# Kernel tuning notes

Hardware: AMD Instinct MI355X
Metric: run time of the kernel (lower is better)

## Reference

```python
import jax, jax.numpy as jnp
import numpy as np

Z_DIM = 128
OUT_DIM = 64
CHANNELS = 3
N_LINEARS = 16
BATCH = 1024
OUT_FEATS = CHANNELS * OUT_DIM * OUT_DIM * N_LINEARS  # 196608


def setup_inputs() -> dict:
    key = jax.random.key(0)
    k_z, k_c, k_w, k_b = jax.random.split(key, 4)
    z = jax.random.normal(k_z, (BATCH, Z_DIM), dtype=jnp.float32)
    # torch.randint(0, n_linears - 1, ...) -> values in [0, 14]
    c = jax.random.randint(k_c, (BATCH,), 0, N_LINEARS - 1, dtype=jnp.int64)
    W = jax.random.normal(k_w, (OUT_FEATS, Z_DIM), dtype=jnp.float32) * 0.02
    b = jax.random.normal(k_b, (OUT_FEATS,), dtype=jnp.float32) * 0.02
    return {"z": z, "c": c, "W": W, "b": b}


def reference(z, c, W, b):
    # Dense linear producing n_linears 'expert' outputs per sample
    out = jnp.einsum('bz,oz->bo', z, W) + b               # [B, O*N]
    out = out.reshape(-1, N_LINEARS, CHANNELS, OUT_DIM, OUT_DIM)
    # Per-sample gather of the selected expert slice
    return out[jnp.arange(out.shape[0]), c]               # [B, C, H, W]
```

## Files before the change

### kernel.cpp

```cpp
#include <hip/hip_runtime.h>


#define Z_DIM  128
#define OPE    12288
#define NEXP   16
#define NT     256
#define NCOLS  128
#define MCHUNK 64
#define WPAD   136

typedef __attribute__((ext_vector_type(8))) short short8;
typedef __attribute__((ext_vector_type(4))) float f32x4;
typedef unsigned short u16;
typedef unsigned int   u32;

__device__ __forceinline__ u16 f2bf(float f) {
    union { float f; u32 u; } a; a.f = f;
    const u32 r = a.u + 0x7FFFu + ((a.u >> 16) & 1u);
    return (u16)(r >> 16);
}

__global__ __launch_bounds__(NT, 6)
void expert_mfma(const float* __restrict__ z,
                 const int* __restrict__ c,
                 const float* __restrict__ W,
                 const float* __restrict__ bias,
                 float* __restrict__ out,
                 int B) {
    __shared__ u16 lst[1024];
    __shared__ int cnt_sh;
    __shared__ __align__(16) u16 Zhi[MCHUNK][WPAD];

    const int tid = threadIdx.x;
    const int e   = blockIdx.y;
    const int n0  = blockIdx.x * NCOLS;

    if (tid == 0) cnt_sh = 0;
    __syncthreads();
    {
        const int4 cv = ((const int4*)c)[tid];
        if (cv.x == e) lst[atomicAdd(&cnt_sh, 1)] = (u16)(tid * 4 + 0);
        if (cv.y == e) lst[atomicAdd(&cnt_sh, 1)] = (u16)(tid * 4 + 1);
        if (cv.z == e) lst[atomicAdd(&cnt_sh, 1)] = (u16)(tid * 4 + 2);
        if (cv.w == e) lst[atomicAdd(&cnt_sh, 1)] = (u16)(tid * 4 + 3);
    }
    __syncthreads();
    const int cnt = cnt_sh;
    if (cnt == 0) return;

    const int lane = tid & 63;
    const int wv   = tid >> 6;
    const int fr   = lane & 15;
    const int kg   = lane >> 4;

    const int col0 = n0 + wv * 16 + fr;
    const int col1 = col0 + 64;
    const float bv0 = bias[(size_t)e * OPE + col0];
    const float bv1 = bias[(size_t)e * OPE + col1];

    short8 bh0[4], bh1[4];
    #pragma unroll
    for (int cg = 0; cg < 2; ++cg) {
        const float* wrow = W + ((size_t)e * OPE + (cg ? col1 : col0)) * Z_DIM;
        #pragma unroll
        for (int kk = 0; kk < 4; ++kk) {
            const float* p = wrow + kk * 32 + kg * 8;
            const float4 v0 = *(const float4*)p;
            const float4 v1 = *(const float4*)(p + 4);
            short8 hh;
            hh[0]=(short)f2bf(v0.x); hh[1]=(short)f2bf(v0.y);
            hh[2]=(short)f2bf(v0.z); hh[3]=(short)f2bf(v0.w);
            hh[4]=(short)f2bf(v1.x); hh[5]=(short)f2bf(v1.y);
            hh[6]=(short)f2bf(v1.z); hh[7]=(short)f2bf(v1.w);
            if (cg) bh1[kk] = hh; else bh0[kk] = hh;
        }
    }

    const int zr = tid >> 2;
    const int zq = (tid & 3) * 32;

    for (int m0 = 0; m0 < cnt; m0 += MCHUNK) {
        __syncthreads();

        const int r = m0 + zr;
        if (r < cnt) {
            const float* zp = z + (size_t)lst[r] * Z_DIM + zq;
            #pragma unroll
            for (int q = 0; q < 4; ++q) {
                const float4 v0 = *(const float4*)(zp + q * 8);
                const float4 v1 = *(const float4*)(zp + q * 8 + 4);
                uint4 hv;
                hv.x = (u32)f2bf(v0.x) | ((u32)f2bf(v0.y) << 16);
                hv.y = (u32)f2bf(v0.z) | ((u32)f2bf(v0.w) << 16);
                hv.z = (u32)f2bf(v1.x) | ((u32)f2bf(v1.y) << 16);
                hv.w = (u32)f2bf(v1.z) | ((u32)f2bf(v1.w) << 16);
                *(uint4*)&Zhi[zr][zq + q * 8] = hv;
            }
        }
        __syncthreads();

        const int mlim = min(cnt - m0, MCHUNK);
        for (int ms = 0; ms < mlim; ms += 16) {
            f32x4 acc0 = {0.f, 0.f, 0.f, 0.f};
            f32x4 acc1 = {0.f, 0.f, 0.f, 0.f};
            #pragma unroll
            for (int kk = 0; kk < 4; ++kk) {
                const short8 ah = *(const short8*)&Zhi[ms + fr][kk * 32 + kg * 8];
                acc0 = __builtin_amdgcn_mfma_f32_16x16x32_bf16(ah, bh0[kk], acc0, 0, 0, 0);
                acc1 = __builtin_amdgcn_mfma_f32_16x16x32_bf16(ah, bh1[kk], acc1, 0, 0, 0);
            }
            #pragma unroll
            for (int j = 0; j < 4; ++j) {
                const int rr = m0 + ms + kg * 4 + j;
                if (rr < cnt) {
                    float* orow = out + (size_t)lst[rr] * OPE;
                    orow[col0] = acc0[j] + bv0;
                    orow[col1] = acc1[j] + bv1;
                }
            }
        }
    }
}

extern "C" void kernel_launch(void* const* d_in, const int* in_sizes, int n_in,
                              void* d_out, int out_size, void* d_ws, size_t ws_size,
                              hipStream_t stream) {
    const float* z = (const float*)d_in[0];
    const int*   c = (const int*)d_in[1];
    const float* W = (const float*)d_in[2];
    const float* b = (const float*)d_in[3];
    float* out = (float*)d_out;
    const int B = in_sizes[0] / Z_DIM;

    dim3 grid(OPE / NCOLS, NEXP);
    expert_mfma<<<grid, NT, 0, stream>>>(z, c, W, b, out, B);
}
```

Before: 172.2 us.

## Precompute per-expert sample lists in a prepass kernel and load Z directly

Adds a single-block prepass kernel that buckets sample indices per expert into workspace, so each GEMM block no longer scans all of c with shared atomics. The main kernel drops the LDS staging of Z and the block barriers, with each lane loading and converting its own Z row fragment straight from global memory into MFMA operands. This trades an extra kernel launch and redundant global Z loads across waves for removing the per-block list build, the synchronisation and the shared memory use.

```diff
diff --git a/kernel.cpp b/kernel.cpp
--- a/kernel.cpp
+++ b/kernel.cpp
@@ -6,8 +6,6 @@
 #define NEXP   16
 #define NT     256
 #define NCOLS  128
-#define MCHUNK 64
-#define WPAD   136
 
 typedef __attribute__((ext_vector_type(8))) short short8;
 typedef __attribute__((ext_vector_type(4))) float f32x4;
@@ -19,35 +17,41 @@
     const u32 r = a.u + 0x7FFFu + ((a.u >> 16) & 1u);
     return (u16)(r >> 16);
 }
+__device__ __forceinline__ u32 pack2(float a, float b) {
+    return (u32)f2bf(a) | ((u32)f2bf(b) << 16);
+}
+union S8 { short8 s; uint4 u; };
+
+__global__ __launch_bounds__(256, 1)
+void build_lists(const int* __restrict__ c, int* __restrict__ ws_cnt,
+                 u16* __restrict__ ws_lst) {
+    __shared__ int cnt_sh[NEXP];
+    const int tid = threadIdx.x;
+    if (tid < NEXP) cnt_sh[tid] = 0;
+    __syncthreads();
+    const int4 cv = ((const int4*)c)[tid];
+    int p;
+    p = atomicAdd(&cnt_sh[cv.x], 1); ws_lst[cv.x * 1024 + p] = (u16)(tid * 4 + 0);
+    p = atomicAdd(&cnt_sh[cv.y], 1); ws_lst[cv.y * 1024 + p] = (u16)(tid * 4 + 1);
+    p = atomicAdd(&cnt_sh[cv.z], 1); ws_lst[cv.z * 1024 + p] = (u16)(tid * 4 + 2);
+    p = atomicAdd(&cnt_sh[cv.w], 1); ws_lst[cv.w * 1024 + p] = (u16)(tid * 4 + 3);
+    __syncthreads();
+    if (tid < NEXP) ws_cnt[tid] = cnt_sh[tid];
+}
 
 __global__ __launch_bounds__(NT, 6)
 void expert_mfma(const float* __restrict__ z,
-                 const int* __restrict__ c,
                  const float* __restrict__ W,
                  const float* __restrict__ bias,
                  float* __restrict__ out,
-                 int B) {
-    __shared__ u16 lst[1024];
-    __shared__ int cnt_sh;
-    __shared__ __align__(16) u16 Zhi[MCHUNK][WPAD];
-
-    const int tid = threadIdx.x;
+                 const int* __restrict__ ws_cnt,
+                 const u16* __restrict__ ws_lst) {
     const int e   = blockIdx.y;
     const int n0  = blockIdx.x * NCOLS;
-
-    if (tid == 0) cnt_sh = 0;
-    __syncthreads();
-    {
-        const int4 cv = ((const int4*)c)[tid];
-        if (cv.x == e) lst[atomicAdd(&cnt_sh, 1)] = (u16)(tid * 4 + 0);
-        if (cv.y == e) lst[atomicAdd(&cnt_sh, 1)] = (u16)(tid * 4 + 1);
-        if (cv.z == e) lst[atomicAdd(&cnt_sh, 1)] = (u16)(tid * 4 + 2);
-        if (cv.w == e) lst[atomicAdd(&cnt_sh, 1)] = (u16)(tid * 4 + 3);
-    }
-    __syncthreads();
-    const int cnt = cnt_sh;
+    const int cnt = ws_cnt[e];
     if (cnt == 0) return;
 
+    const int tid  = threadIdx.x;
     const int lane = tid & 63;
     const int wv   = tid >> 6;
     const int fr   = lane & 15;
@@ -57,6 +61,7 @@
     const int col1 = col0 + 64;
     const float bv0 = bias[(size_t)e * OPE + col0];
     const float bv1 = bias[(size_t)e * OPE + col1];
+    const u16* lst  = ws_lst + e * 1024;
 
     short8 bh0[4], bh1[4];
     #pragma unroll
@@ -67,56 +72,37 @@
             const float* p = wrow + kk * 32 + kg * 8;
             const float4 v0 = *(const float4*)p;
             const float4 v1 = *(const float4*)(p + 4);
-            short8 hh;
-            hh[0]=(short)f2bf(v0.x); hh[1]=(short)f2bf(v0.y);
-            hh[2]=(short)f2bf(v0.z); hh[3]=(short)f2bf(v0.w);
-            hh[4]=(short)f2bf(v1.x); hh[5]=(short)f2bf(v1.y);
-            hh[6]=(short)f2bf(v1.z); hh[7]=(short)f2bf(v1.w);
-            if (cg) bh1[kk] = hh; else bh0[kk] = hh;
+            S8 h;
+            h.u.x = pack2(v0.x, v0.y); h.u.y = pack2(v0.z, v0.w);
+            h.u.z = pack2(v1.x, v1.y); h.u.w = pack2(v1.z, v1.w);
+            if (cg) bh1[kk] = h.s; else bh0[kk] = h.s;
         }
     }
 
-    const int zr = tid >> 2;
-    const int zq = (tid & 3) * 32;
+    for (int ms = 0; ms < cnt; ms += 16) {
+        const int r = min(ms + fr, cnt - 1);
+        const float* zp = z + (size_t)lst[r] * Z_DIM;
 
-    for (int m0 = 0; m0 < cnt; m0 += MCHUNK) {
-        __syncthreads();
-
-        const int r = m0 + zr;
-        if (r < cnt) {
-            const float* zp = z + (size_t)lst[r] * Z_DIM + zq;
-            #pragma unroll
-            for (int q = 0; q < 4; ++q) {
-                const float4 v0 = *(const float4*)(zp + q * 8);
-                const float4 v1 = *(const float4*)(zp + q * 8 + 4);
-                uint4 hv;
-                hv.x = (u32)f2bf(v0.x) | ((u32)f2bf(v0.y) << 16);
-                hv.y = (u32)f2bf(v0.z) | ((u32)f2bf(v0.w) << 16);
-                hv.z = (u32)f2bf(v1.x) | ((u32)f2bf(v1.y) << 16);
-                hv.w = (u32)f2bf(v1.z) | ((u32)f2bf(v1.w) << 16);
-                *(uint4*)&Zhi[zr][zq + q * 8] = hv;
-            }
+        f32x4 acc0 = {0.f, 0.f, 0.f, 0.f};
+        f32x4 acc1 = {0.f, 0.f, 0.f, 0.f};
+        #pragma unroll
+        for (int kk = 0; kk < 4; ++kk) {
+            const float* p = zp + kk * 32 + kg * 8;
+            const float4 v0 = *(const float4*)p;
+            const float4 v1 = *(const float4*)(p + 4);
+            S8 a;
+            a.u.x = pack2(v0.x, v0.y); a.u.y = pack2(v0.z, v0.w);
+            a.u.z = pack2(v1.x, v1.y); a.u.w = pack2(v1.z, v1.w);
+            acc0 = __builtin_amdgcn_mfma_f32_16x16x32_bf16(a.s, bh0[kk], acc0, 0, 0, 0);
+            acc1 = __builtin_amdgcn_mfma_f32_16x16x32_bf16(a.s, bh1[kk], acc1, 0, 0, 0);
         }
-        __syncthreads();
-
-        const int mlim = min(cnt - m0, MCHUNK);
-        for (int ms = 0; ms < mlim; ms += 16) {
-            f32x4 acc0 = {0.f, 0.f, 0.f, 0.f};
-            f32x4 acc1 = {0.f, 0.f, 0.f, 0.f};
-            #pragma unroll
-            for (int kk = 0; kk < 4; ++kk) {
-                const short8 ah = *(const short8*)&Zhi[ms + fr][kk * 32 + kg * 8];
-                acc0 = __builtin_amdgcn_mfma_f32_16x16x32_bf16(ah, bh0[kk], acc0, 0, 0, 0);
-                acc1 = __builtin_amdgcn_mfma_f32_16x16x32_bf16(ah, bh1[kk], acc1, 0, 0, 0);
-            }
-            #pragma unroll
-            for (int j = 0; j < 4; ++j) {
-                const int rr = m0 + ms + kg * 4 + j;
-                if (rr < cnt) {
-                    float* orow = out + (size_t)lst[rr] * OPE;
-                    orow[col0] = acc0[j] + bv0;
-                    orow[col1] = acc1[j] + bv1;
-                }
+        #pragma unroll
+        for (int j = 0; j < 4; ++j) {
+            const int rr = ms + kg * 4 + j;
+            if (rr < cnt) {
+                float* orow = out + (size_t)lst[rr] * OPE;
+                orow[col0] = acc0[j] + bv0;
+                orow[col1] = acc1[j] + bv1;
             }
         }
     }
@@ -130,8 +116,12 @@
     const float* W = (const float*)d_in[2];
     const float* b = (const float*)d_in[3];
     float* out = (float*)d_out;
-    const int B = in_sizes[0] / Z_DIM;
+
+    int* ws_cnt = (int*)d_ws;
+    u16* ws_lst = (u16*)((char*)d_ws + 64);
+
+    build_lists<<<1, 256, 0, stream>>>(c, ws_cnt, ws_lst);
 
     dim3 grid(OPE / NCOLS, NEXP);
-    expert_mfma<<<grid, NT, 0, stream>>>(z, c, W, b, out, B);
+    expert_mfma<<<grid, NT, 0, stream>>>(z, W, b, out, ws_cnt, ws_lst);
 }
```

Result: slower. 188.6 us (+9.6%).
